# Performance work log

Measured on AMD Instinct MI355X. Metric: run time of the kernel, lower is better.

Reference implementation:

```python
import jax, jax.numpy as jnp
import numpy as np

B, L, D, K = 32, 512, 512, 3
LOG_2PI = float(np.log(2.0 * np.pi))


def conv1d(x, w, b):
    # x: (B, L, 1), w: (D, 1, K), b: (D,) -> (B, L, D); padding = (K-1)//2
    pad = (w.shape[-1] - 1) // 2
    y = jax.lax.conv_general_dilated(
        x.transpose(0, 2, 1), w, window_strides=(1,), padding=[(pad, pad)],
        dimension_numbers=('NCH', 'OIH', 'NCH'))
    return y.transpose(0, 2, 1) + b


def setup_inputs() -> dict:
    ks = jax.random.split(jax.random.key(0), 14)
    x = jax.random.normal(ks[0], (B, L, D), dtype=jnp.float32)
    durations_float = jax.random.uniform(ks[1], (B, L), dtype=jnp.float32) * 8.0
    durations_int = jax.random.randint(ks[2], (B, L), 1, 8, dtype=jnp.int32)
    energies = jax.random.normal(ks[3], (B, L), dtype=jnp.float32)
    pitch = jax.random.normal(ks[4], (B, L), dtype=jnp.float32)
    input_lengths = jax.random.randint(ks[5], (B,), L // 2, L + 1, dtype=jnp.int32)
    input_lengths = input_lengths.at[0].set(L)  # ensure max length == L (torch masks at max(lengths))
    s = 0.05
    w_dur = jax.random.normal(ks[6], (D, 1, K), dtype=jnp.float32) * s
    b_dur = jax.random.normal(ks[7], (D,), dtype=jnp.float32) * s
    w_en = jax.random.normal(ks[8], (D, 1, K), dtype=jnp.float32) * s
    b_en = jax.random.normal(ks[9], (D,), dtype=jnp.float32) * s
    w_pitch = jax.random.normal(ks[10], (D, 1, K), dtype=jnp.float32) * s
    b_pitch = jax.random.normal(ks[11], (D,), dtype=jnp.float32) * s
    w_lin = jax.random.normal(ks[12], (1, D), dtype=jnp.float32) * s
    b_lin = jax.random.normal(ks[13], (1,), dtype=jnp.float32) * s
    nb_frames = int(jnp.max(jnp.cumsum(durations_int, axis=1)))  # concrete static T
    return dict(x=x, durations_float=durations_float, durations_int=durations_int,
                energies=energies, pitch=pitch, input_lengths=input_lengths,
                w_dur=w_dur, b_dur=b_dur, w_en=w_en, b_en=b_en,
                w_pitch=w_pitch, b_pitch=b_pitch, w_lin=w_lin, b_lin=b_lin,
                nb_frames=nb_frames)


def reference(x, durations_float, durations_int, energies, pitch, input_lengths,
              w_dur, b_dur, w_en, b_en, w_pitch, b_pitch, w_lin, b_lin, nb_frames):
    Bb, Ll, Dd = x.shape
    dur_e = conv1d(durations_float[..., None], w_dur, b_dur)   # (B, L, D)
    en_e = conv1d(energies[..., None], w_en, b_en)
    pi_e = conv1d(pitch[..., None], w_pitch, b_pitch)
    x = x + en_e + pi_e
    range_inputs = x + dur_e
    ranges = jax.nn.softplus(range_inputs @ w_lin.T + b_lin)[..., 0]  # (B, L)
    valid = jnp.arange(Ll) < input_lengths[:, None]                   # (B, L) True = valid
    ranges = jnp.where(valid, ranges, 1.0)
    d = durations_int.astype(x.dtype)
    cumsum = jnp.cumsum(durations_int, axis=1)
    means = d * 0.5 + jnp.concatenate(
        [jnp.zeros((Bb, 1), x.dtype), cumsum[:, :-1].astype(x.dtype)], axis=1)  # (B, L)
    frames = jnp.arange(nb_frames, dtype=x.dtype) + 0.5                # (T,)
    z = (frames[None, None, :] - means[..., None]) / ranges[..., None] # (B, L, T)
    log_probs = -0.5 * z * z - jnp.log(ranges)[..., None] - 0.5 * LOG_2PI
    probs = jnp.where(valid[..., None], jnp.exp(log_probs), 0.0)       # (B, L, T)
    weights = probs / (jnp.sum(probs, axis=1, keepdims=True) + 1e-20)
    # torch: sum_L x[b,l,d] * w[b,l,t] -> (B, D, T), then permute -> (B, T, D)
    x_upsamp = jnp.einsum('bld,blt->btd', x, weights)
    return x_upsamp, weights
```

## Files before the change

### kernel.cpp

```cpp
#include <hip/hip_runtime.h>
#include <hip/hip_bf16.h>
#include <stdint.h>

#define NB 32
#define NL 512
#define ND 512

typedef __bf16 bf16x8 __attribute__((ext_vector_type(8)));
typedef float  f32x4  __attribute__((ext_vector_type(4)));

__device__ __forceinline__ unsigned short f2bf(float f) {
    uint32_t u = __float_as_uint(f);
    u = (u + 0x7fffu + ((u >> 16) & 1u)) >> 16;
    return (unsigned short)u;
}


__global__ __launch_bounds__(256) void fuse2_kernel(
    const float* __restrict__ x, const float* __restrict__ df,
    const float* __restrict__ en, const float* __restrict__ pi,
    const int* __restrict__ lens,
    const float* __restrict__ w_dur, const float* __restrict__ b_dur,
    const float* __restrict__ w_en,  const float* __restrict__ b_en,
    const float* __restrict__ w_pi,  const float* __restrict__ b_pi,
    const float* __restrict__ w_lin, const float* __restrict__ b_lin,
    unsigned short* __restrict__ Xb, float* __restrict__ ranges)
{
    const int blk = blockIdx.x;
    const int b   = blk >> 6;
    const int lb  = (blk & 63) << 3;
    const int tid = threadIdx.x;
    const int d0  = tid << 1;

    float we[2][3], wp[2][3], wd[2][3], bev[2], bpv[2], bdv[2], wl[2];
    #pragma unroll
    for (int q = 0; q < 2; ++q) {
        const int d = d0 + q;
        #pragma unroll
        for (int k = 0; k < 3; ++k) {
            we[q][k] = w_en[d*3+k];
            wp[q][k] = w_pi[d*3+k];
            wd[q][k] = w_dur[d*3+k];
        }
        bev[q] = b_en[d]; bpv[q] = b_pi[d]; bdv[q] = b_dur[d]; wl[q] = w_lin[d];
    }

    float acc[8];
    #pragma unroll
    for (int i = 0; i < 8; ++i) acc[i] = 0.f;

    uint4 chunk[2];
    unsigned short* cu = (unsigned short*)chunk;

    #pragma unroll
    for (int li = 0; li < 8; ++li) {
        const int l  = lb + li;
        const int bl = (b << 9) + l;
        const float dm1 = (l > 0)      ? df[bl-1] : 0.f;
        const float dc  = df[bl];
        const float dp1 = (l < NL-1)   ? df[bl+1] : 0.f;
        const float em1 = (l > 0)      ? en[bl-1] : 0.f;
        const float ec  = en[bl];
        const float ep1 = (l < NL-1)   ? en[bl+1] : 0.f;
        const float pm1 = (l > 0)      ? pi[bl-1] : 0.f;
        const float pc  = pi[bl];
        const float pp1 = (l < NL-1)   ? pi[bl+1] : 0.f;
        const float2 xv = *(const float2*)&x[(size_t)bl * ND + d0];
        #pragma unroll
        for (int q = 0; q < 2; ++q) {
            const float ev  = we[q][0]*em1 + we[q][1]*ec + we[q][2]*ep1 + bev[q];
            const float pv  = wp[q][0]*pm1 + wp[q][1]*pc + wp[q][2]*pp1 + bpv[q];
            const float xxv = (q ? xv.y : xv.x) + ev + pv;
            cu[q*8 + li] = f2bf(xxv);
            const float dv  = wd[q][0]*dm1 + wd[q][1]*dc + wd[q][2]*dp1 + bdv[q];
            acc[li] += (xxv + dv) * wl[q];
        }
    }
    #pragma unroll
    for (int q = 0; q < 2; ++q) {
        const int d = d0 + q;
        const size_t off = (size_t)b * (NL * ND)
            + (size_t)(((lb >> 5) << 5) + (d >> 4)) * 512
            + (size_t)((((lb >> 3) & 3) << 4) + (d & 15)) * 8;
        *(uint4*)&Xb[off] = chunk[q];
    }

    #pragma unroll
    for (int li = 0; li < 8; ++li)
        #pragma unroll
        for (int off = 32; off; off >>= 1)
            acc[li] += __shfl_down(acc[li], off, 64);
    __shared__ float red[4][8];
    const int lane = tid & 63, wid = tid >> 6;
    if (lane == 0)
        #pragma unroll
        for (int li = 0; li < 8; ++li) red[wid][li] = acc[li];
    __syncthreads();
    if (tid < 8) {
        const float s = red[0][tid] + red[1][tid] + red[2][tid] + red[3][tid] + b_lin[0];
        float r = fmaxf(s, 0.f) + log1pf(expf(-fabsf(s)));
        if (lb + tid >= lens[b]) r = 1.0f;
        ranges[(b << 9) + lb + tid] = r;
    }
}


#define STAGE_X(kk, buf) do {                                                   \
    const char* src_ = Bbase + (size_t)(kk) * 32768;                            \
    _Pragma("unroll")                                                           \
    for (int c = 0; c < 4; ++c) {                                               \
        const int base = (wid * 64 + c * 512) * 16;                             \
        __builtin_amdgcn_global_load_lds(                                       \
            (__attribute__((address_space(1))) void*)(src_ + base + lane * 16), \
            (__attribute__((address_space(3))) void*)(ldsX[buf] + base), 16, 0, 0); \
    }                                                                           \
} while (0)

#define GENP(kk, buf) do {                                                      \
    const int l0_ = (kk) * 32 + oct * 8;                                        \
    float pv_[8]; uint4 pk_; unsigned short* pu_ = (unsigned short*)&pk_;       \
    _Pragma("unroll")                                                           \
    for (int j = 0; j < 8; ++j) {                                               \
        const float zz = fmaf(ftv, t_sinv[l0_ + j], t_nms[l0_ + j]);            \
        pv_[j] = t_sc[l0_ + j] * __expf(-0.5f * zz * zz);                       \
        pu_[j] = f2bf(pv_[j]);                                                  \
    }                                                                           \
    if (tvalid) {                                                               \
        _Pragma("unroll")                                                       \
        for (int j = 0; j < 8; ++j)                                             \
            wout[((size_t)(b << 9) + l0_ + j) * T + tglb] = pv_[j] * myDinv;    \
    }                                                                           \
    *(uint4*)(ldsP[buf] + mbP * 1024 + (oct * 16 + (tloc & 15)) * 16) = pk_;    \
} while (0)

__global__ __launch_bounds__(512, 2) void fusedwg_kernel(
    const unsigned short* __restrict__ Xb,
    const float* __restrict__ ranges, const int* __restrict__ di,
    const int* __restrict__ lens,
    float* __restrict__ wout, float* __restrict__ xup, int T)
{
    __shared__ __align__(16) char ldsP[2][8192];
    __shared__ __align__(16) char ldsX[2][32768];
    __shared__ float t_sinv[NL], t_nms[NL], t_sc[NL];
    __shared__ float partial[4][128];
    __shared__ float dinvL[128];
    __shared__ int scanA[NL], scanB[NL];

    const int tid  = threadIdx.x;
    const int lane = tid & 63, wid = tid >> 6;
    const int wm = wid >> 2, wn = wid & 3;

    const int i    = blockIdx.x;
    const int xcd  = i & 7, slot = i >> 3;
    const int b    = (xcd << 2) + (slot & 3);
    const int m    = slot >> 2;

    const int tloc = tid & 127;
    const int oct  = tid >> 7;
    const int mbP  = tloc >> 4;
    const int tglb = m * 128 + tloc;
    const bool tvalid = tglb < T;
    const float ftv = (float)tglb + 0.5f;

    const int dv = di[(b << 9) + tid];
    scanA[tid] = dv;
    __syncthreads();
    {
        int* src = scanA; int* dst = scanB;
        #pragma unroll
        for (int off = 1; off < NL; off <<= 1) {
            dst[tid] = src[tid] + (tid >= off ? src[tid - off] : 0);
            __syncthreads();
            int* tmp = src; src = dst; dst = tmp;
        }
        const float mu = (float)src[tid] - 0.5f * (float)dv;
        const float r  = ranges[(b << 9) + tid];
        const float inv = 1.f / r;
        t_sinv[tid] = inv;
        t_nms[tid]  = -mu * inv;
        t_sc[tid]   = (tid < lens[b]) ? 0.3989422804014327f * inv : 0.f;
    }
    __syncthreads();

    {
        float s = 0.f;
        const int lbeg = oct * 128;
        #pragma unroll 4
        for (int l = lbeg; l < lbeg + 128; ++l) {
            const float zz = fmaf(ftv, t_sinv[l], t_nms[l]);
            s += t_sc[l] * __expf(-0.5f * zz * zz);
        }
        partial[oct][tloc] = s;
    }
    __syncthreads();
    if (tid < 128) {
        const float sum = partial[0][tid] + partial[1][tid] + partial[2][tid] + partial[3][tid];
        dinvL[tid] = (m * 128 + tid < T) ? 1.f / (sum + 1e-20f) : 0.f;
    }
    __syncthreads();
    const float myDinv = dinvL[tloc];

    const char* Bbase = (const char*)Xb + (size_t)b * (NL * ND * 2);

    f32x4 acc[4][8];
    #pragma unroll
    for (int ii = 0; ii < 4; ++ii)
        #pragma unroll
        for (int jj = 0; jj < 8; ++jj) acc[ii][jj] = (f32x4){0.f, 0.f, 0.f, 0.f};

    STAGE_X(0, 0);
    GENP(0, 0);

    for (int k = 0; k < 16; ++k) {
        const int cur = k & 1;
        __syncthreads();
        if (k < 15) {
            STAGE_X(k + 1, cur ^ 1);
            GENP(k + 1, cur ^ 1);
        }
        bf16x8 af[4], bfr[8];
        #pragma unroll
        for (int ii = 0; ii < 4; ++ii)
            af[ii] = *(const bf16x8*)(ldsP[cur] + ((wm << 2) + ii) * 1024 + lane * 16);
        #pragma unroll
        for (int jj = 0; jj < 8; ++jj)
            bfr[jj] = *(const bf16x8*)(ldsX[cur] + ((wn << 3) + jj) * 1024 + lane * 16);
        #pragma unroll
        for (int ii = 0; ii < 4; ++ii)
            #pragma unroll
            for (int jj = 0; jj < 8; ++jj)
                acc[ii][jj] = __builtin_amdgcn_mfma_f32_16x16x32_bf16(af[ii], bfr[jj], acc[ii][jj], 0, 0, 0);
    }

    const int d_base = (wn << 7) + (lane & 15);
    float* Ob = xup + (size_t)b * T * ND;
    #pragma unroll
    for (int ii = 0; ii < 4; ++ii) {
        #pragma unroll
        for (int r = 0; r < 4; ++r) {
            const int tl2 = (wm << 6) + ii * 16 + ((lane >> 4) << 2) + r;
            const int t = m * 128 + tl2;
            if (t < T) {
                const float dsc = dinvL[tl2];
                #pragma unroll
                for (int jj = 0; jj < 8; ++jj)
                    Ob[(size_t)t * ND + d_base + jj * 16] = acc[ii][jj][r] * dsc;
            }
        }
    }
}

__global__ __launch_bounds__(512) void means_kernel(
    const int* __restrict__ di, float* __restrict__ means)
{
    const int b = blockIdx.x;
    const int l = threadIdx.x;
    __shared__ int s[NL];
    const int d = di[b * NL + l];
    s[l] = d;
    __syncthreads();
    #pragma unroll
    for (int off = 1; off < NL; off <<= 1) {
        const int v = (l >= off) ? s[l - off] : 0;
        __syncthreads();
        s[l] += v;
        __syncthreads();
    }
    means[b * NL + l] = 0.5f * (float)d + (float)(s[l] - d);
}

__global__ __launch_bounds__(256) void fuse_kernel(
    const float* __restrict__ x, const float* __restrict__ df,
    const float* __restrict__ en, const float* __restrict__ pi,
    const int* __restrict__ lens,
    const float* __restrict__ w_dur, const float* __restrict__ b_dur,
    const float* __restrict__ w_en,  const float* __restrict__ b_en,
    const float* __restrict__ w_pi,  const float* __restrict__ b_pi,
    const float* __restrict__ w_lin, const float* __restrict__ b_lin,
    float* __restrict__ xx, float* __restrict__ ranges)
{
    const int bl = blockIdx.x;
    const int b  = bl >> 9;
    const int l  = bl & (NL - 1);
    const int tid = threadIdx.x;
    const float dm1 = (l > 0)      ? df[bl - 1] : 0.f;
    const float d0  = df[bl];
    const float dp1 = (l < NL - 1) ? df[bl + 1] : 0.f;
    const float em1 = (l > 0)      ? en[bl - 1] : 0.f;
    const float e0  = en[bl];
    const float ep1 = (l < NL - 1) ? en[bl + 1] : 0.f;
    const float pm1 = (l > 0)      ? pi[bl - 1] : 0.f;
    const float p0  = pi[bl];
    const float pp1 = (l < NL - 1) ? pi[bl + 1] : 0.f;
    float acc = 0.f;
    #pragma unroll
    for (int d = tid; d < ND; d += 256) {
        const float xv = x[(size_t)bl * ND + d];
        const float ev = w_en[d*3]*em1 + w_en[d*3+1]*e0 + w_en[d*3+2]*ep1 + b_en[d];
        const float pv = w_pi[d*3]*pm1 + w_pi[d*3+1]*p0 + w_pi[d*3+2]*pp1 + b_pi[d];
        const float xxv = xv + ev + pv;
        xx[(size_t)bl * ND + d] = xxv;
        const float dv = w_dur[d*3]*dm1 + w_dur[d*3+1]*d0 + w_dur[d*3+2]*dp1 + b_dur[d];
        acc += (xxv + dv) * w_lin[d];
    }
    #pragma unroll
    for (int off = 32; off; off >>= 1) acc += __shfl_down(acc, off, 64);
    __shared__ float red[4];
    const int lane = tid & 63, wid = tid >> 6;
    if (lane == 0) red[wid] = acc;
    __syncthreads();
    if (tid == 0) {
        const float s = red[0] + red[1] + red[2] + red[3] + b_lin[0];
        float r = fmaxf(s, 0.f) + log1pf(expf(-fabsf(s)));
        if (l >= lens[b]) r = 1.0f;
        ranges[bl] = r;
    }
}

__global__ __launch_bounds__(256) void weights_kernel(
    const float* __restrict__ ranges, const float* __restrict__ means,
    const int* __restrict__ lens, float* __restrict__ weights, int T)
{
    const int b = blockIdx.y;
    const int t = blockIdx.x * 256 + threadIdx.x;
    __shared__ float sm[NL], sinv[NL], sc[NL];
    const int len = lens[b];
    for (int l = threadIdx.x; l < NL; l += 256) {
        const float r = ranges[b * NL + l];
        const float inv = 1.f / r;
        sm[l] = means[b * NL + l];
        sinv[l] = inv;
        sc[l] = (l < len) ? 0.3989422804014327f * inv : 0.f;
    }
    __syncthreads();
    if (t >= T) return;
    const float ft = (float)t + 0.5f;
    float sum = 0.f;
    #pragma unroll 4
    for (int l = 0; l < NL; ++l) {
        const float z = (ft - sm[l]) * sinv[l];
        sum += sc[l] * __expf(-0.5f * z * z);
    }
    const float dinv = 1.f / (sum + 1e-20f);
    #pragma unroll 4
    for (int l = 0; l < NL; ++l) {
        const float z = (ft - sm[l]) * sinv[l];
        weights[((size_t)b * NL + l) * T + t] = sc[l] * __expf(-0.5f * z * z) * dinv;
    }
}

#define BM 64
#define BN 64
#define BK 16
__global__ __launch_bounds__(256) void gemm_f32_kernel(
    const float* __restrict__ xx, const float* __restrict__ weights,
    float* __restrict__ out, int T)
{
    const int b  = blockIdx.z;
    const int t0 = blockIdx.y * BM;
    const int d0 = blockIdx.x * BN;
    const float* __restrict__ W = weights + (size_t)b * NL * T;
    const float* __restrict__ X = xx + (size_t)b * NL * ND;
    float* __restrict__ O = out + (size_t)b * T * ND;
    __shared__ float As[BK][BM];
    __shared__ float Bs[BK][BN];
    const int tid = threadIdx.x;
    const int tx = tid & 15;
    const int ty = tid >> 4;
    const int lr = tid >> 4;
    const int lc = (tid & 15) * 4;
    const bool vec_ok = (t0 + BM <= T) && ((T & 3) == 0);
    float acc[4][4] = {};
    for (int l0 = 0; l0 < NL; l0 += BK) {
        if (vec_ok) {
            *(float4*)&As[lr][lc] = *(const float4*)&W[(size_t)(l0 + lr) * T + t0 + lc];
        } else {
            #pragma unroll
            for (int j = 0; j < 4; ++j) {
                const int tcol = t0 + lc + j;
                As[lr][lc + j] = (tcol < T) ? W[(size_t)(l0 + lr) * T + tcol] : 0.f;
            }
        }
        *(float4*)&Bs[lr][lc] = *(const float4*)&X[(size_t)(l0 + lr) * ND + d0 + lc];
        __syncthreads();
        #pragma unroll
        for (int k = 0; k < BK; ++k) {
            float a[4], bb[4];
            *(float4*)a  = *(const float4*)&As[k][ty * 4];
            *(float4*)bb = *(const float4*)&Bs[k][tx * 4];
            #pragma unroll
            for (int i = 0; i < 4; ++i)
                #pragma unroll
                for (int j = 0; j < 4; ++j)
                    acc[i][j] += a[i] * bb[j];
        }
        __syncthreads();
    }
    #pragma unroll
    for (int i = 0; i < 4; ++i) {
        const int t = t0 + ty * 4 + i;
        if (t < T)
            *(float4*)&O[(size_t)t * ND + d0 + tx * 4] =
                make_float4(acc[i][0], acc[i][1], acc[i][2], acc[i][3]);
    }
}

extern "C" void kernel_launch(void* const* d_in, const int* in_sizes, int n_in,
                              void* d_out, int out_size, void* d_ws, size_t ws_size,
                              hipStream_t stream) {
    const float* x     = (const float*)d_in[0];
    const float* df    = (const float*)d_in[1];
    const int*   di    = (const int*)  d_in[2];
    const float* en    = (const float*)d_in[3];
    const float* pi    = (const float*)d_in[4];
    const int*   lens  = (const int*)  d_in[5];
    const float* w_dur = (const float*)d_in[6];
    const float* b_dur = (const float*)d_in[7];
    const float* w_en  = (const float*)d_in[8];
    const float* b_en  = (const float*)d_in[9];
    const float* w_pi  = (const float*)d_in[10];
    const float* b_pi  = (const float*)d_in[11];
    const float* w_lin = (const float*)d_in[12];
    const float* b_lin = (const float*)d_in[13];

    const int B = NB, L = NL, D = ND;
    const int T = out_size / (B * (L + D));
    const int MT = (T + 127) / 128;

    float* xup  = (float*)d_out;
    float* wout = xup + (size_t)B * T * D;

    const size_t XbBytes = (size_t)B * L * D * 2;
    const size_t need = XbBytes + (size_t)B * L * sizeof(float);

    if (ws_size >= need) {
        unsigned short* Xb = (unsigned short*)d_ws;
        float* ranges = (float*)(Xb + (size_t)B * L * D);

        hipLaunchKernelGGL(fuse2_kernel, dim3(B * 64), dim3(256), 0, stream,
                           x, df, en, pi, lens, w_dur, b_dur, w_en, b_en,
                           w_pi, b_pi, w_lin, b_lin, Xb, ranges);
        hipLaunchKernelGGL(fusedwg_kernel, dim3(MT * 32), dim3(512), 0, stream,
                           Xb, ranges, di, lens, wout, xup, T);
    } else {
        float* xx     = (float*)d_ws;
        float* ranges = xx + (size_t)B * L * D;
        float* means  = ranges + (size_t)B * L;
        hipLaunchKernelGGL(fuse_kernel, dim3(B * L), dim3(256), 0, stream,
                           x, df, en, pi, lens, w_dur, b_dur, w_en, b_en,
                           w_pi, b_pi, w_lin, b_lin, xx, ranges);
        hipLaunchKernelGGL(means_kernel, dim3(B), dim3(512), 0, stream, di, means);
        hipLaunchKernelGGL(weights_kernel, dim3((T + 255) / 256, B), dim3(256), 0, stream,
                           ranges, means, lens, wout, T);
        hipLaunchKernelGGL(gemm_f32_kernel, dim3(D / BN, (T + BM - 1) / BM, B), dim3(256), 0, stream,
                           xx, wout, xup, T);
    }
}
```

Baseline: 122.7 us.

## Halve T-tile to 64 rows, overlay LDS, and stage epilogue through shared memory

The fused weights-plus-GEMM kernel now tiles 64 frames per block instead of 128, with each of the 8 waves owning a 64-column D slice. Shared memory is overlaid into one buffer and occupancy is raised to 4 blocks per CU. The output is transposed through LDS so rows are written as coalesced float4 stores, and explicit waitcnt/barrier control replaces __syncthreads in the main loop. The smaller tile doubles the grid and recomputes the per-block scan and normalisation sums more often, and each wave now has fewer MFMAs per LDS load.

```diff
diff --git a/kernel.cpp b/kernel.cpp
--- a/kernel.cpp
+++ b/kernel.cpp
@@ -105,60 +105,66 @@
 }
 
 
-#define STAGE_X(kk, buf) do {                                                   \
+#define STAGE_X2(kk, buf) do {                                                  \
     const char* src_ = Bbase + (size_t)(kk) * 32768;                            \
+    char* dst_ = smem + (buf) * 32768;                                          \
     _Pragma("unroll")                                                           \
     for (int c = 0; c < 4; ++c) {                                               \
-        const int base = (wid * 64 + c * 512) * 16;                             \
+        const int o_ = (wid * 4 + c) * 1024;                                    \
         __builtin_amdgcn_global_load_lds(                                       \
-            (__attribute__((address_space(1))) void*)(src_ + base + lane * 16), \
-            (__attribute__((address_space(3))) void*)(ldsX[buf] + base), 16, 0, 0); \
+            (__attribute__((address_space(1))) void*)(src_ + o_ + lane * 16),   \
+            (__attribute__((address_space(3))) void*)(dst_ + o_), 16, 0, 0);    \
     }                                                                           \
 } while (0)
 
-#define GENP(kk, buf) do {                                                      \
-    const int l0_ = (kk) * 32 + oct * 8;                                        \
-    float pv_[8]; uint4 pk_; unsigned short* pu_ = (unsigned short*)&pk_;       \
+#define GENP2(kk, buf) do {                                                     \
+    const int l0_ = (kk) * 32 + oct * 4;                                        \
+    float pv_[4];                                                               \
+    unsigned short pu_[4];                                                      \
     _Pragma("unroll")                                                           \
-    for (int j = 0; j < 8; ++j) {                                               \
+    for (int j = 0; j < 4; ++j) {                                               \
         const float zz = fmaf(ftv, t_sinv[l0_ + j], t_nms[l0_ + j]);            \
         pv_[j] = t_sc[l0_ + j] * __expf(-0.5f * zz * zz);                       \
         pu_[j] = f2bf(pv_[j]);                                                  \
     }                                                                           \
+    char* pd_ = smem + 65536 + (buf) * 4096 + (tloc >> 4) * 1024               \
+              + (((oct >> 1) << 4) + (tloc & 15)) * 16 + ((oct & 1) << 3);      \
+    *(uint2*)pd_ = *(uint2*)pu_;                                                \
     if (tvalid) {                                                               \
         _Pragma("unroll")                                                       \
-        for (int j = 0; j < 8; ++j)                                             \
+        for (int j = 0; j < 4; ++j)                                             \
             wout[((size_t)(b << 9) + l0_ + j) * T + tglb] = pv_[j] * myDinv;    \
     }                                                                           \
-    *(uint4*)(ldsP[buf] + mbP * 1024 + (oct * 16 + (tloc & 15)) * 16) = pk_;    \
 } while (0)
 
-__global__ __launch_bounds__(512, 2) void fusedwg_kernel(
+__global__ __launch_bounds__(512, 4) void fusedwg2_kernel(
     const unsigned short* __restrict__ Xb,
     const float* __restrict__ ranges, const int* __restrict__ di,
     const int* __restrict__ lens,
     float* __restrict__ wout, float* __restrict__ xup, int T)
 {
-    __shared__ __align__(16) char ldsP[2][8192];
-    __shared__ __align__(16) char ldsX[2][32768];
-    __shared__ float t_sinv[NL], t_nms[NL], t_sc[NL];
-    __shared__ float partial[4][128];
-    __shared__ float dinvL[128];
-    __shared__ int scanA[NL], scanB[NL];
+    __shared__ __align__(16) char smem[80128];
+    float* t_sinv = (float*)(smem + 73728);
+    float* t_nms  = (float*)(smem + 75776);
+    float* t_sc   = (float*)(smem + 77824);
+    float* dinvL  = (float*)(smem + 79872);
+    int*   scanA  = (int*)smem;
+    int*   scanB  = (int*)(smem + 2048);
+    float* partial = (float*)(smem + 4096);
 
     const int tid  = threadIdx.x;
     const int lane = tid & 63, wid = tid >> 6;
-    const int wm = wid >> 2, wn = wid & 3;
+    const int wn   = wid;
 
     const int i    = blockIdx.x;
     const int xcd  = i & 7, slot = i >> 3;
     const int b    = (xcd << 2) + (slot & 3);
     const int m    = slot >> 2;
-
-    const int tloc = tid & 127;
-    const int oct  = tid >> 7;
-    const int mbP  = tloc >> 4;
-    const int tglb = m * 128 + tloc;
+    const int m64  = m << 6;
+
+    const int tloc = tid & 63;
+    const int oct  = tid >> 6;
+    const int tglb = m64 + tloc;
     const bool tvalid = tglb < T;
     const float ftv = (float)tglb + 0.5f;
 
@@ -184,67 +190,85 @@
 
     {
         float s = 0.f;
-        const int lbeg = oct * 128;
+        const int lbeg = oct << 6;
         #pragma unroll 4
-        for (int l = lbeg; l < lbeg + 128; ++l) {
+        for (int l = lbeg; l < lbeg + 64; ++l) {
             const float zz = fmaf(ftv, t_sinv[l], t_nms[l]);
             s += t_sc[l] * __expf(-0.5f * zz * zz);
         }
-        partial[oct][tloc] = s;
-    }
-    __syncthreads();
-    if (tid < 128) {
-        const float sum = partial[0][tid] + partial[1][tid] + partial[2][tid] + partial[3][tid];
-        dinvL[tid] = (m * 128 + tid < T) ? 1.f / (sum + 1e-20f) : 0.f;
+        partial[(oct << 6) + tloc] = s;
+    }
+    __syncthreads();
+    if (tid < 64) {
+        float sum = 0.f;
+        #pragma unroll
+        for (int o = 0; o < 8; ++o) sum += partial[(o << 6) + tid];
+        dinvL[tid] = 1.f / (sum + 1e-20f);
     }
     __syncthreads();
     const float myDinv = dinvL[tloc];
 
     const char* Bbase = (const char*)Xb + (size_t)b * (NL * ND * 2);
 
-    f32x4 acc[4][8];
+    f32x4 acc[4][4];
     #pragma unroll
     for (int ii = 0; ii < 4; ++ii)
         #pragma unroll
-        for (int jj = 0; jj < 8; ++jj) acc[ii][jj] = (f32x4){0.f, 0.f, 0.f, 0.f};
-
-    STAGE_X(0, 0);
-    GENP(0, 0);
+        for (int jj = 0; jj < 4; ++jj) acc[ii][jj] = (f32x4){0.f, 0.f, 0.f, 0.f};
+
+    STAGE_X2(0, 0);
+    __builtin_amdgcn_sched_barrier(0);
+    GENP2(0, 0);
 
     for (int k = 0; k < 16; ++k) {
+        asm volatile("s_waitcnt vmcnt(4) lgkmcnt(0)" ::: "memory");
+        __builtin_amdgcn_s_barrier();
+        __builtin_amdgcn_sched_barrier(0);
         const int cur = k & 1;
-        __syncthreads();
         if (k < 15) {
-            STAGE_X(k + 1, cur ^ 1);
-            GENP(k + 1, cur ^ 1);
-        }
-        bf16x8 af[4], bfr[8];
+            STAGE_X2(k + 1, cur ^ 1);
+            __builtin_amdgcn_sched_barrier(0);
+            GENP2(k + 1, cur ^ 1);
+        }
+        bf16x8 af[4], bfr[4];
         #pragma unroll
         for (int ii = 0; ii < 4; ++ii)
-            af[ii] = *(const bf16x8*)(ldsP[cur] + ((wm << 2) + ii) * 1024 + lane * 16);
-        #pragma unroll
-        for (int jj = 0; jj < 8; ++jj)
-            bfr[jj] = *(const bf16x8*)(ldsX[cur] + ((wn << 3) + jj) * 1024 + lane * 16);
+            af[ii] = *(const bf16x8*)(smem + 65536 + cur * 4096 + ii * 1024 + lane * 16);
+        #pragma unroll
+        for (int jj = 0; jj < 4; ++jj)
+            bfr[jj] = *(const bf16x8*)(smem + cur * 32768 + ((wn << 2) + jj) * 1024 + lane * 16);
         #pragma unroll
         for (int ii = 0; ii < 4; ++ii)
             #pragma unroll
-            for (int jj = 0; jj < 8; ++jj)
+            for (int jj = 0; jj < 4; ++jj)
                 acc[ii][jj] = __builtin_amdgcn_mfma_f32_16x16x32_bf16(af[ii], bfr[jj], acc[ii][jj], 0, 0, 0);
     }
 
-    const int d_base = (wn << 7) + (lane & 15);
+    float* lf = (float*)smem;
     float* Ob = xup + (size_t)b * T * ND;
     #pragma unroll
-    for (int ii = 0; ii < 4; ++ii) {
-        #pragma unroll
-        for (int r = 0; r < 4; ++r) {
-            const int tl2 = (wm << 6) + ii * 16 + ((lane >> 4) << 2) + r;
-            const int t = m * 128 + tl2;
+    for (int c = 0; c < 4; ++c) {
+        __syncthreads();
+        #pragma unroll
+        for (int jj = 0; jj < 4; ++jj)
+            #pragma unroll
+            for (int r = 0; r < 4; ++r) {
+                const int row = ((lane >> 4) << 2) + r;
+                const int col = (wn << 6) + (jj << 4) + (lane & 15);
+                lf[row * 516 + col] = acc[c][jj][r];
+            }
+        __syncthreads();
+        const int trow = tid >> 7;
+        const int colq = (tid & 127) << 2;
+        #pragma unroll
+        for (int s = 0; s < 4; ++s) {
+            const int row = trow + (s << 2);
+            const int t = m64 + (c << 4) + row;
             if (t < T) {
-                const float dsc = dinvL[tl2];
-                #pragma unroll
-                for (int jj = 0; jj < 8; ++jj)
-                    Ob[(size_t)t * ND + d_base + jj * 16] = acc[ii][jj][r] * dsc;
+                const float dsc = dinvL[(c << 4) + row];
+                f32x4 v = *(const f32x4*)(lf + row * 516 + colq);
+                v[0] *= dsc; v[1] *= dsc; v[2] *= dsc; v[3] *= dsc;
+                *(f32x4*)&Ob[(size_t)t * ND + colq] = v;
             }
         }
     }
@@ -425,7 +449,7 @@
 
     const int B = NB, L = NL, D = ND;
     const int T = out_size / (B * (L + D));
-    const int MT = (T + 127) / 128;
+    const int MT = (T + 63) / 64;
 
     float* xup  = (float*)d_out;
     float* wout = xup + (size_t)B * T * D;
@@ -440,7 +464,7 @@
         hipLaunchKernelGGL(fuse2_kernel, dim3(B * 64), dim3(256), 0, stream,
                            x, df, en, pi, lens, w_dur, b_dur, w_en, b_en,
                            w_pi, b_pi, w_lin, b_lin, Xb, ranges);
-        hipLaunchKernelGGL(fusedwg_kernel, dim3(MT * 32), dim3(512), 0, stream,
+        hipLaunchKernelGGL(fusedwg2_kernel, dim3(MT * 32), dim3(512), 0, stream,
                            Xb, ranges, di, lens, wout, xup, T);
     } else {
         float* xx     = (float*)d_ws;
```

Result: faster. 101.5 us (-17.3%).
